# Performance work log

Hardware: AMD Instinct MI355X
Metric: run time of the kernel (lower is better)

The kernel has to match this reference:

```python
import jax, jax.numpy as jnp
import numpy as np

N_NODES = 100000
N_EDGES = 3200000
IN_CH = 128
OUT_CH = 64


def gcn_conv(x, src, dst, W, b, n):
    """PyG GCNConv: out = D^{-1/2} (A+I) D^{-1/2} (x @ W) + b.
    src/dst already include self-loops. Aggregation at dst (source_to_target)."""
    deg = jax.ops.segment_sum(jnp.ones_like(dst, x.dtype), dst, num_segments=n)  # [N]
    dinv = jnp.where(deg > 0, jax.lax.rsqrt(deg), 0.0)
    norm = dinv[src] * dinv[dst]                     # [E+N]
    xw = x @ W                                       # [N, out] dense GEMM first (PyG order)
    msgs = xw[src] * norm[:, None]                   # gather + scale, [E+N, out]
    return jax.ops.segment_sum(msgs, dst, num_segments=n) + b


def setup_inputs() -> dict:
    key = jax.random.key(0)
    ks = jax.random.split(key, 6)
    x = jax.random.normal(ks[0], (N_NODES, IN_CH), dtype=jnp.float32)
    edge_index = jax.random.randint(ks[1], (2, N_EDGES), 0, N_NODES, dtype=jnp.int32)
    # Glorot-style init for GCNConv weights
    W1 = jax.random.normal(ks[2], (IN_CH, IN_CH), dtype=jnp.float32) * (1.0 / np.sqrt(IN_CH))
    b1 = jnp.zeros((IN_CH,), dtype=jnp.float32)
    W2 = jax.random.normal(ks[3], (IN_CH, OUT_CH), dtype=jnp.float32) * (1.0 / np.sqrt(IN_CH))
    b2 = jnp.zeros((OUT_CH,), dtype=jnp.float32)
    return {"x": x, "edge_index": edge_index, "W1": W1, "b1": b1, "W2": W2, "b2": b2}


def reference(x, edge_index, W1, b1, W2, b2):
    n = x.shape[0]
    loop = jnp.arange(n, dtype=edge_index.dtype)
    src = jnp.concatenate([edge_index[0], loop])  # add self-loops once; reused by both layers
    dst = jnp.concatenate([edge_index[1], loop])
    h = jax.nn.sigmoid(gcn_conv(x, src, dst, W1, b1, n))
    return jax.nn.sigmoid(gcn_conv(h, src, dst, W2, b2, n))
```

## Files before the change

kernel.cpp:

```cpp
#include <hip/hip_runtime.h>
#include <hip/hip_bf16.h>
#include <hip/hip_fp16.h>

#define IN_CH 128
#define NODES_PER_BUCKET 128
#define BUCKET_CAP 5120
#define EPB 8192

using f32x2 = __attribute__((ext_vector_type(2))) float;
using f32x4 = __attribute__((ext_vector_type(4))) float;
using f16x8 = __attribute__((ext_vector_type(8))) _Float16;
using i32x4 = __attribute__((ext_vector_type(4))) int;

__device__ __forceinline__ float sigmoidf_(float x) { return 1.0f / (1.0f + __expf(-x)); }
__device__ __forceinline__ __half2 u2h(unsigned u) { return __builtin_bit_cast(__half2, u); }
__device__ __forceinline__ unsigned packh2(float a, float b) {
    return __builtin_bit_cast(unsigned, __float22half2_rn(make_float2(a, b)));
}

#if __has_builtin(__builtin_amdgcn_cvt_pk_f32_fp8) && __has_builtin(__builtin_amdgcn_cvt_pk_fp8_f32)
#define FP8_HW 1
#else
#define FP8_HW 0
__device__ __forceinline__ unsigned fp8_enc1(float f) {
    unsigned short us = __builtin_bit_cast(unsigned short, __float2half(f));
    unsigned s = (us >> 8) & 0x80u;
    unsigned mag = us & 0x7fffu;
    if (mag < 0x2400u) return s;
    unsigned t = mag - 0x2000u;
    t += 0x3Fu + ((t >> 7) & 1u);
    unsigned r = t >> 7;
    if (r > 0x7Eu) r = 0x7Eu;
    return s | r;
}
__device__ __forceinline__ float fp8_dec1(unsigned v) {
    unsigned s = (v & 0x80u) << 8;
    unsigned m = v & 0x7Fu;
    unsigned h = m ? (((m << 7) + 0x2000u) | s) : s;
    return __half2float(__builtin_bit_cast(__half, (unsigned short)h));
}
#endif

__device__ __forceinline__ void acc16(float* a, uint4 v) {
#if FP8_HW
    f32x2 t;
    t = __builtin_amdgcn_cvt_pk_f32_fp8(v.x, false); a[0] += t[0];  a[1] += t[1];
    t = __builtin_amdgcn_cvt_pk_f32_fp8(v.x, true);  a[2] += t[0];  a[3] += t[1];
    t = __builtin_amdgcn_cvt_pk_f32_fp8(v.y, false); a[4] += t[0];  a[5] += t[1];
    t = __builtin_amdgcn_cvt_pk_f32_fp8(v.y, true);  a[6] += t[0];  a[7] += t[1];
    t = __builtin_amdgcn_cvt_pk_f32_fp8(v.z, false); a[8] += t[0];  a[9] += t[1];
    t = __builtin_amdgcn_cvt_pk_f32_fp8(v.z, true);  a[10] += t[0]; a[11] += t[1];
    t = __builtin_amdgcn_cvt_pk_f32_fp8(v.w, false); a[12] += t[0]; a[13] += t[1];
    t = __builtin_amdgcn_cvt_pk_f32_fp8(v.w, true);  a[14] += t[0]; a[15] += t[1];
#else
    unsigned d[4] = {v.x, v.y, v.z, v.w};
#pragma unroll
    for (int q = 0; q < 4; q++)
#pragma unroll
        for (int b = 0; b < 4; b++) a[q * 4 + b] += fp8_dec1((d[q] >> (8 * b)) & 0xffu);
#endif
}

__device__ __forceinline__ unsigned pack4fp8(float a, float b, float c, float d) {
#if FP8_HW
    unsigned r = 0;
    r = __builtin_amdgcn_cvt_pk_fp8_f32(a, b, r, false);
    r = __builtin_amdgcn_cvt_pk_fp8_f32(c, d, r, true);
    return r;
#else
    return fp8_enc1(a) | (fp8_enc1(b) << 8) | (fp8_enc1(c) << 16) | (fp8_enc1(d) << 24);
#endif
}

__global__ __launch_bounds__(256) void k_bucket_scatter(const int* __restrict__ src,
                                                        const int* __restrict__ dst, int E,
                                                        int* __restrict__ bucketCnt, int NB,
                                                        unsigned* __restrict__ pairBuf) {
    __shared__ int hist[1024];
    int tid = threadIdx.x;
    for (int t = tid; t < 1024; t += 256) hist[t] = 0;
    __syncthreads();
    int base = blockIdx.x * EPB;
    int end = min(base + EPB, E);
    int cnt = end - base;
    int cnt4 = cnt >> 2;
    const i32x4* d4 = (const i32x4*)(dst + base);
    const i32x4* s4 = (const i32x4*)(src + base);

    unsigned pr[8][4];
    unsigned rkb[8][4];
#pragma unroll
    for (int j = 0; j < 8; j++) {
        int i = tid + j * 256;
        if (i < cnt4) {
            i32x4 d = __builtin_nontemporal_load(d4 + i);
            i32x4 s = __builtin_nontemporal_load(s4 + i);
            int b, r;
            b = d[0] >> 7; r = atomicAdd(&hist[b], 1);
            pr[j][0] = ((unsigned)s[0] << 7) | (unsigned)(d[0] & 127); rkb[j][0] = ((unsigned)r << 10) | (unsigned)b;
            b = d[1] >> 7; r = atomicAdd(&hist[b], 1);
            pr[j][1] = ((unsigned)s[1] << 7) | (unsigned)(d[1] & 127); rkb[j][1] = ((unsigned)r << 10) | (unsigned)b;
            b = d[2] >> 7; r = atomicAdd(&hist[b], 1);
            pr[j][2] = ((unsigned)s[2] << 7) | (unsigned)(d[2] & 127); rkb[j][2] = ((unsigned)r << 10) | (unsigned)b;
            b = d[3] >> 7; r = atomicAdd(&hist[b], 1);
            pr[j][3] = ((unsigned)s[3] << 7) | (unsigned)(d[3] & 127); rkb[j][3] = ((unsigned)r << 10) | (unsigned)b;
        }
    }
    unsigned prT = 0, rkbT = 0;
    bool hasT = false;
    {
        int tl = cnt & 3;
        if (tid < tl) {
            int i = base + (cnt4 << 2) + tid;
            int d = dst[i];
            int b = d >> 7;
            int r = atomicAdd(&hist[b], 1);
            prT = ((unsigned)src[i] << 7) | (unsigned)(d & 127);
            rkbT = ((unsigned)r << 10) | (unsigned)b;
            hasT = true;
        }
    }
    __syncthreads();
    for (int t = tid; t < NB; t += 256) {
        int c = hist[t];
        hist[t] = c ? atomicAdd(&bucketCnt[t], c) : 0;
    }
    __syncthreads();
#pragma unroll
    for (int j = 0; j < 8; j++) {
        int i = tid + j * 256;
        if (i < cnt4) {
#pragma unroll
            for (int q = 0; q < 4; q++) {
                unsigned t = rkb[j][q];
                int b = (int)(t & 1023u);
                int pos = hist[b] + (int)(t >> 10);
                if (pos < BUCKET_CAP) pairBuf[(size_t)b * BUCKET_CAP + pos] = pr[j][q];
            }
        }
    }
    if (hasT) {
        int b = (int)(rkbT & 1023u);
        int pos = hist[b] + (int)(rkbT >> 10);
        if (pos < BUCKET_CAP) pairBuf[(size_t)b * BUCKET_CAP + pos] = prT;
    }
}

__global__ __launch_bounds__(1024) void k_scan_buckets(const int* __restrict__ bucketCnt, int NB,
                                                       int* __restrict__ bucketBase,
                                                       int* __restrict__ rowptr, int n) {
    __shared__ int sh[1024];
    int t = threadIdx.x;
    int v = (t < NB) ? min(bucketCnt[t], BUCKET_CAP) : 0;
    sh[t] = v;
    __syncthreads();
    for (int off = 1; off < 1024; off <<= 1) {
        int u = (t >= off) ? sh[t - off] : 0;
        __syncthreads();
        sh[t] += u;
        __syncthreads();
    }
    if (t < NB) bucketBase[t] = sh[t] - v;
    if (t == 1023) rowptr[n] = sh[1023];
}

__global__ __launch_bounds__(256) void k_bucket_place2(const unsigned* __restrict__ pairBuf,
                                                       const int* __restrict__ bucketCnt,
                                                       const int* __restrict__ bucketBase,
                                                       int* __restrict__ rowptr,
                                                       float* __restrict__ dinv,
                                                       int* __restrict__ col, int n) {
    __shared__ int hist[NODES_PER_BUCKET];
    __shared__ int excl[NODES_PER_BUCKET];
    __shared__ int stage[BUCKET_CAP];
    int b = blockIdx.x;
    int tid = threadIdx.x;
    int first = b * NODES_PER_BUCKET;
    if (tid < NODES_PER_BUCKET) hist[tid] = 0;
    __syncthreads();
    int cb = min(bucketCnt[b], BUCKET_CAP);
    const unsigned* p = pairBuf + (size_t)b * BUCKET_CAP;
    for (int e = tid; e < cb; e += 256) atomicAdd(&hist[p[e] & 127], 1);
    __syncthreads();
    int v = (tid < NODES_PER_BUCKET) ? hist[tid] : 0;
    if (tid < NODES_PER_BUCKET) excl[tid] = v;
    __syncthreads();
    for (int off = 1; off < NODES_PER_BUCKET; off <<= 1) {
        int u = (tid < NODES_PER_BUCKET && tid >= off) ? excl[tid - off] : 0;
        __syncthreads();
        if (tid < NODES_PER_BUCKET) excl[tid] += u;
        __syncthreads();
    }
    int base = bucketBase[b];
    if (tid < NODES_PER_BUCKET) {
        int node = first + tid;
        int ex = excl[tid] - v;
        if (node < n) {
            rowptr[node] = base + ex;
            dinv[node] = rsqrtf((float)(v + 1));
        }
        hist[tid] = ex;
    }
    __syncthreads();
    for (int e = tid; e < cb; e += 256) {
        unsigned pr = p[e];
        int lpos = atomicAdd(&hist[pr & 127], 1);
        stage[lpos] = (int)(pr >> 7);
    }
    __syncthreads();
    for (int i = tid; i < cb; i += 256) col[base + i] = stage[i];
}

__global__ __launch_bounds__(256) void k_wprep(const float* __restrict__ W1,
                                               const float* __restrict__ W2,
                                               _Float16* __restrict__ wT1,
                                               _Float16* __restrict__ wT2) {
    int i = blockIdx.x * 256 + threadIdx.x;
    if (i < 128 * 128) {
        int nn = i >> 7, k = i & 127;
        wT1[i] = (_Float16)W1[k * 128 + nn];
    }
    if (i < 64 * 128) {
        int nn = i >> 7, k = i & 127;
        wT2[i] = (_Float16)W2[k * 64 + nn];
    }
}

template <int OUTC, bool INHALF>
__global__ __launch_bounds__(256) void k_gemm_mfma(const void* __restrict__ Xv,
                                                   const _Float16* __restrict__ wT,
                                                   const float* __restrict__ dinv,
                                                   unsigned char* __restrict__ Yb, int n) {
    constexpr int NT = OUTC / 16;
    int tid = threadIdx.x;
    int wave = tid >> 6;
    int lane = tid & 63;
    int tx = lane & 15;
    int q = lane >> 4;
    int r0 = blockIdx.x * 64 + wave * 16;
    int m = r0 + tx;
    int mc = min(m, n - 1);

    f32x4 acc[NT];
#pragma unroll
    for (int nt = 0; nt < NT; nt++) acc[nt] = (f32x4)(0.0f);

#pragma unroll
    for (int ks = 0; ks < 4; ks++) {
        int k0 = ks * 32 + q * 8;
        f16x8 bfrag;
        if constexpr (INHALF) {
            bfrag = *(const f16x8*)((const _Float16*)Xv + (size_t)mc * 128 + k0);
        } else {
            const float* xr = (const float*)Xv + (size_t)mc * 128 + k0;
            float4 x0 = *(const float4*)xr;
            float4 x1 = *(const float4*)(xr + 4);
            bfrag[0] = (_Float16)x0.x; bfrag[1] = (_Float16)x0.y;
            bfrag[2] = (_Float16)x0.z; bfrag[3] = (_Float16)x0.w;
            bfrag[4] = (_Float16)x1.x; bfrag[5] = (_Float16)x1.y;
            bfrag[6] = (_Float16)x1.z; bfrag[7] = (_Float16)x1.w;
        }
#pragma unroll
        for (int nt = 0; nt < NT; nt++) {
            f16x8 afrag = *(const f16x8*)(wT + (size_t)(nt * 16 + tx) * 128 + k0);
            acc[nt] = __builtin_amdgcn_mfma_f32_16x16x32_f16(afrag, bfrag, acc[nt], 0, 0, 0);
        }
    }
    if (m < n) {
        float dv = dinv[m];
        unsigned char* yrow = Yb + (size_t)m * OUTC;
#pragma unroll
        for (int nt = 0; nt < NT; nt++) {
            unsigned d = pack4fp8(acc[nt][0] * dv, acc[nt][1] * dv, acc[nt][2] * dv, acc[nt][3] * dv);
            *(unsigned*)(yrow + nt * 16 + q * 4) = d;
        }
    }
}

template <int C, bool OUTHALF>
__global__ __launch_bounds__(256) void k_agg(const uint4* __restrict__ Y4,
                                             const int* __restrict__ rowptr,
                                             const int* __restrict__ col,
                                             const float* __restrict__ dinv,
                                             const float* __restrict__ bias,
                                             void* __restrict__ out, int n, int zidx) {
    constexpr int LPE = C / 16;
    constexpr int NPW = 64 / LPE;
    constexpr int RS = C / 16;
    int gid = blockIdx.x * blockDim.x + threadIdx.x;
    int wid = gid >> 6;
    int lane = gid & 63;
    int g = lane / LPE;
    int sub = lane % LPE;
    int node = wid * NPW + g;
    bool valid = node < n;
    int nc = valid ? node : 0;
    int s0 = rowptr[nc];
    int s1 = valid ? rowptr[nc + 1] : s0;

    float a0[16];
#pragma unroll
    for (int k = 0; k < 16; k++) a0[k] = 0.f;

    {
        int idx = valid ? node : zidx;
        uint4 v = Y4[(size_t)idx * RS + sub];
        acc16(a0, v);
    }
    int e = s0;
    for (; e + 8 <= s1; e += 8) {
        int c0 = __builtin_nontemporal_load(col + e);
        int c1 = __builtin_nontemporal_load(col + e + 1);
        int c2 = __builtin_nontemporal_load(col + e + 2);
        int c3 = __builtin_nontemporal_load(col + e + 3);
        int c4 = __builtin_nontemporal_load(col + e + 4);
        int c5 = __builtin_nontemporal_load(col + e + 5);
        int c6 = __builtin_nontemporal_load(col + e + 6);
        int c7 = __builtin_nontemporal_load(col + e + 7);
        uint4 v0 = Y4[(size_t)c0 * RS + sub];
        uint4 v1 = Y4[(size_t)c1 * RS + sub];
        uint4 v2 = Y4[(size_t)c2 * RS + sub];
        uint4 v3 = Y4[(size_t)c3 * RS + sub];
        uint4 v4 = Y4[(size_t)c4 * RS + sub];
        uint4 v5 = Y4[(size_t)c5 * RS + sub];
        uint4 v6 = Y4[(size_t)c6 * RS + sub];
        uint4 v7 = Y4[(size_t)c7 * RS + sub];
        acc16(a0, v0);
        acc16(a0, v1);
        acc16(a0, v2);
        acc16(a0, v3);
        acc16(a0, v4);
        acc16(a0, v5);
        acc16(a0, v6);
        acc16(a0, v7);
    }
    if (e < s1) {
        int i0 = min(e + 0, s1 - 1), i1 = min(e + 1, s1 - 1);
        int i2 = min(e + 2, s1 - 1), i3 = min(e + 3, s1 - 1);
        int i4 = min(e + 4, s1 - 1), i5 = min(e + 5, s1 - 1);
        int i6 = min(e + 6, s1 - 1), i7 = min(e + 7, s1 - 1);
        int c0 = (e + 0 < s1) ? col[i0] : zidx;
        int c1 = (e + 1 < s1) ? col[i1] : zidx;
        int c2 = (e + 2 < s1) ? col[i2] : zidx;
        int c3 = (e + 3 < s1) ? col[i3] : zidx;
        int c4 = (e + 4 < s1) ? col[i4] : zidx;
        int c5 = (e + 5 < s1) ? col[i5] : zidx;
        int c6 = (e + 6 < s1) ? col[i6] : zidx;
        int c7 = (e + 7 < s1) ? col[i7] : zidx;
        uint4 v0 = Y4[(size_t)c0 * RS + sub];
        uint4 v1 = Y4[(size_t)c1 * RS + sub];
        uint4 v2 = Y4[(size_t)c2 * RS + sub];
        uint4 v3 = Y4[(size_t)c3 * RS + sub];
        uint4 v4 = Y4[(size_t)c4 * RS + sub];
        uint4 v5 = Y4[(size_t)c5 * RS + sub];
        uint4 v6 = Y4[(size_t)c6 * RS + sub];
        uint4 v7 = Y4[(size_t)c7 * RS + sub];
        acc16(a0, v0);
        acc16(a0, v1);
        acc16(a0, v2);
        acc16(a0, v3);
        acc16(a0, v4);
        acc16(a0, v5);
        acc16(a0, v6);
        acc16(a0, v7);
    }

    if (valid) {
        float dv = dinv[node];
        float4 bv[4];
        bv[0] = *(const float4*)&bias[sub * 16];
        bv[1] = *(const float4*)&bias[sub * 16 + 4];
        bv[2] = *(const float4*)&bias[sub * 16 + 8];
        bv[3] = *(const float4*)&bias[sub * 16 + 12];
        float o[16];
#pragma unroll
        for (int q = 0; q < 4; q++) {
            const float* bq = (const float*)&bv[q];
#pragma unroll
            for (int b = 0; b < 4; b++) o[q * 4 + b] = sigmoidf_(a0[q * 4 + b] * dv + bq[b]);
        }
        if constexpr (OUTHALF) {
            constexpr int OR = C / 8;
            uint4 h0, h1;
            h0.x = packh2(o[0], o[1]);   h0.y = packh2(o[2], o[3]);
            h0.z = packh2(o[4], o[5]);   h0.w = packh2(o[6], o[7]);
            h1.x = packh2(o[8], o[9]);   h1.y = packh2(o[10], o[11]);
            h1.z = packh2(o[12], o[13]); h1.w = packh2(o[14], o[15]);
            ((uint4*)out)[(size_t)node * OR + sub * 2] = h0;
            ((uint4*)out)[(size_t)node * OR + sub * 2 + 1] = h1;
        } else {
            float* op = (float*)out + (size_t)node * C + sub * 16;
            f32x4 o0 = {o[0], o[1], o[2], o[3]};
            f32x4 o1 = {o[4], o[5], o[6], o[7]};
            f32x4 o2 = {o[8], o[9], o[10], o[11]};
            f32x4 o3 = {o[12], o[13], o[14], o[15]};
            __builtin_nontemporal_store(o0, (f32x4*)(op + 0));
            __builtin_nontemporal_store(o1, (f32x4*)(op + 4));
            __builtin_nontemporal_store(o2, (f32x4*)(op + 8));
            __builtin_nontemporal_store(o3, (f32x4*)(op + 12));
        }
    }
}

extern "C" void kernel_launch(void* const* d_in, const int* in_sizes, int n_in,
                              void* d_out, int out_size, void* d_ws, size_t ws_size,
                              hipStream_t stream) {
    const float* x  = (const float*)d_in[0];
    const int* eidx = (const int*)d_in[1];
    const float* W1 = (const float*)d_in[2];
    const float* b1 = (const float*)d_in[3];
    const float* W2 = (const float*)d_in[4];
    const float* b2 = (const float*)d_in[5];
    float* out = (float*)d_out;

    int n = in_sizes[0] / IN_CH;
    int E = in_sizes[1] / 2;
    const int* srcv = eidx;
    const int* dstv = eidx + E;
    int NB = (n + NODES_PER_BUCKET - 1) / NODES_PER_BUCKET;

    char* w = (char*)d_ws;
    auto alloc = [&](size_t bytes) {
        char* p = w;
        w += (bytes + 255) & ~(size_t)255;
        return p;
    };
    int* bucketCnt      = (int*)alloc((size_t)NB * 4);
    int* bucketBase     = (int*)alloc((size_t)NB * 4);
    unsigned* pairBuf   = (unsigned*)alloc((size_t)NB * BUCKET_CAP * 4);
    int* rowptr         = (int*)alloc(((size_t)n + 1) * 4);
    float* dinv         = (float*)alloc((size_t)n * 4);
    int* col            = (int*)alloc((size_t)E * 4);
    unsigned char* y    = (unsigned char*)alloc(((size_t)n + 1) * 128);
    unsigned short* h   = (unsigned short*)alloc((size_t)n * IN_CH * 2);
    _Float16* wT1       = (_Float16*)alloc(128 * 128 * 2);
    _Float16* wT2       = (_Float16*)alloc(64 * 128 * 2);

    hipMemsetAsync(bucketCnt, 0, (size_t)NB * 4, stream);
    hipMemsetAsync(y + (size_t)n * 128, 0, 128, stream);

    k_wprep<<<64, 256, 0, stream>>>(W1, W2, wT1, wT2);
    int nblk = (E + EPB - 1) / EPB;
    k_bucket_scatter<<<nblk, 256, 0, stream>>>(srcv, dstv, E, bucketCnt, NB, pairBuf);
    k_scan_buckets<<<1, 1024, 0, stream>>>(bucketCnt, NB, bucketBase, rowptr, n);
    k_bucket_place2<<<NB, 256, 0, stream>>>(pairBuf, bucketCnt, bucketBase, rowptr, dinv, col, n);

    int gemmGrid = (n + 63) / 64;

    k_gemm_mfma<128, false><<<gemmGrid, 256, 0, stream>>>(x, wT1, dinv, y, n);
    k_agg<128, true><<<(n + 31) / 32, 256, 0, stream>>>((const uint4*)y, rowptr, col, dinv, b1, h, n, n);
    k_gemm_mfma<64, true><<<gemmGrid, 256, 0, stream>>>(h, wT2, dinv, y, n);
    k_agg<64, false><<<(n + 63) / 64, 256, 0, stream>>>((const uint4*)y, rowptr, col, dinv, b2, out, n, 2 * n);
}
```

Measured before the change: 235.8 us.

## Sort nodes by degree within buckets to balance aggregation wavefronts

Computes a per-bucket permutation of nodes ordered by in-degree inside the CSR placement kernel and has the aggregation kernels process nodes in that order, so node groups sharing a wavefront have similar edge counts and less divergence. It also swaps nontemporal col loads for normal loads. This adds an O(128) rank loop per node and an extra perm indirection, and output writes become scattered within each bucket.

Result: no change. 235.1 us (-0.3%).

```diff
diff --git a/kernel.cpp b/kernel.cpp
--- a/kernel.cpp
+++ b/kernel.cpp
@@ -169,9 +169,11 @@
                                                        const int* __restrict__ bucketBase,
                                                        int* __restrict__ rowptr,
                                                        float* __restrict__ dinv,
-                                                       int* __restrict__ col, int n) {
+                                                       int* __restrict__ col,
+                                                       int* __restrict__ perm, int n) {
     __shared__ int hist[NODES_PER_BUCKET];
     __shared__ int excl[NODES_PER_BUCKET];
+    __shared__ int degs[NODES_PER_BUCKET];
     __shared__ int stage[BUCKET_CAP];
     int b = blockIdx.x;
     int tid = threadIdx.x;
@@ -183,7 +185,10 @@
     for (int e = tid; e < cb; e += 256) atomicAdd(&hist[p[e] & 127], 1);
     __syncthreads();
     int v = (tid < NODES_PER_BUCKET) ? hist[tid] : 0;
-    if (tid < NODES_PER_BUCKET) excl[tid] = v;
+    if (tid < NODES_PER_BUCKET) {
+        excl[tid] = v;
+        degs[tid] = (first + tid < n) ? v : 0x7fffffff;
+    }
     __syncthreads();
     for (int off = 1; off < NODES_PER_BUCKET; off <<= 1) {
         int u = (tid < NODES_PER_BUCKET && tid >= off) ? excl[tid - off] : 0;
@@ -209,6 +214,19 @@
     }
     __syncthreads();
     for (int i = tid; i < cb; i += 256) col[base + i] = stage[i];
+    if (tid < NODES_PER_BUCKET) {
+        int node = first + tid;
+        if (node < n) {
+            int myd = degs[tid];
+            int rank = 0;
+#pragma unroll 8
+            for (int j = 0; j < NODES_PER_BUCKET; j++) {
+                int dj = degs[j];
+                rank += (dj < myd) || (dj == myd && j < tid);
+            }
+            perm[first + rank] = node;
+        }
+    }
 }
 
 __global__ __launch_bounds__(256) void k_wprep(const float* __restrict__ W1,
@@ -281,6 +299,7 @@
 __global__ __launch_bounds__(256) void k_agg(const uint4* __restrict__ Y4,
                                              const int* __restrict__ rowptr,
                                              const int* __restrict__ col,
+                                             const int* __restrict__ perm,
                                              const float* __restrict__ dinv,
                                              const float* __restrict__ bias,
                                              void* __restrict__ out, int n, int zidx) {
@@ -292,11 +311,11 @@
     int lane = gid & 63;
     int g = lane / LPE;
     int sub = lane % LPE;
-    int node = wid * NPW + g;
-    bool valid = node < n;
-    int nc = valid ? node : 0;
-    int s0 = rowptr[nc];
-    int s1 = valid ? rowptr[nc + 1] : s0;
+    int pidx = wid * NPW + g;
+    bool valid = pidx < n;
+    int node = valid ? perm[pidx] : 0;
+    int s0 = rowptr[node];
+    int s1 = valid ? rowptr[node + 1] : s0;
 
     float a0[16];
 #pragma unroll
@@ -309,14 +328,14 @@
     }
     int e = s0;
     for (; e + 8 <= s1; e += 8) {
-        int c0 = __builtin_nontemporal_load(col + e);
-        int c1 = __builtin_nontemporal_load(col + e + 1);
-        int c2 = __builtin_nontemporal_load(col + e + 2);
-        int c3 = __builtin_nontemporal_load(col + e + 3);
-        int c4 = __builtin_nontemporal_load(col + e + 4);
-        int c5 = __builtin_nontemporal_load(col + e + 5);
-        int c6 = __builtin_nontemporal_load(col + e + 6);
-        int c7 = __builtin_nontemporal_load(col + e + 7);
+        int c0 = col[e];
+        int c1 = col[e + 1];
+        int c2 = col[e + 2];
+        int c3 = col[e + 3];
+        int c4 = col[e + 4];
+        int c5 = col[e + 5];
+        int c6 = col[e + 6];
+        int c7 = col[e + 7];
         uint4 v0 = Y4[(size_t)c0 * RS + sub];
         uint4 v1 = Y4[(size_t)c1 * RS + sub];
         uint4 v2 = Y4[(size_t)c2 * RS + sub];
@@ -431,6 +450,7 @@
     int* rowptr         = (int*)alloc(((size_t)n + 1) * 4);
     float* dinv         = (float*)alloc((size_t)n * 4);
     int* col            = (int*)alloc((size_t)E * 4);
+    int* perm           = (int*)alloc((size_t)n * 4);
     unsigned char* y    = (unsigned char*)alloc(((size_t)n + 1) * 128);
     unsigned short* h   = (unsigned short*)alloc((size_t)n * IN_CH * 2);
     _Float16* wT1       = (_Float16*)alloc(128 * 128 * 2);
@@ -443,12 +463,12 @@
     int nblk = (E + EPB - 1) / EPB;
     k_bucket_scatter<<<nblk, 256, 0, stream>>>(srcv, dstv, E, bucketCnt, NB, pairBuf);
     k_scan_buckets<<<1, 1024, 0, stream>>>(bucketCnt, NB, bucketBase, rowptr, n);
-    k_bucket_place2<<<NB, 256, 0, stream>>>(pairBuf, bucketCnt, bucketBase, rowptr, dinv, col, n);
+    k_bucket_place2<<<NB, 256, 0, stream>>>(pairBuf, bucketCnt, bucketBase, rowptr, dinv, col, perm, n);
 
     int gemmGrid = (n + 63) / 64;
 
     k_gemm_mfma<128, false><<<gemmGrid, 256, 0, stream>>>(x, wT1, dinv, y, n);
-    k_agg<128, true><<<(n + 31) / 32, 256, 0, stream>>>((const uint4*)y, rowptr, col, dinv, b1, h, n, n);
+    k_agg<128, true><<<(n + 31) / 32, 256, 0, stream>>>((const uint4*)y, rowptr, col, perm, dinv, b1, h, n, n);
     k_gemm_mfma<64, true><<<gemmGrid, 256, 0, stream>>>(h, wT2, dinv, y, n);
-    k_agg<64, false><<<(n + 63) / 64, 256, 0, stream>>>((const uint4*)y, rowptr, col, dinv, b2, out, n, 2 * n);
-}
+    k_agg<64, false><<<(n + 63) / 64, 256, 0, stream>>>((const uint4*)y, rowptr, col, perm, dinv, b2, out, n, 2 * n);
+}
```
